# Kernel tuning notes

Measured on AMD Instinct MI355X. Metric: run time of the kernel, lower is better.

## Reference

```python
import jax, jax.numpy as jnp
import numpy as np

B, T = 64, 1000
RNN_DIM, EMB_DIM, ATT_DIM, LOC_DIM, KSIZE = 1024, 512, 128, 32, 31


def setup_inputs() -> dict:
    key = jax.random.key(0)
    ks = jax.random.split(key, 8)
    s = 0.02  # small init scale for weights
    return {
        "attention_hidden_state": jax.random.normal(ks[0], (B, RNN_DIM), jnp.float32),
        "memory": jax.random.normal(ks[1], (B, T, EMB_DIM), jnp.float32),
        "processed_memory": jax.random.normal(ks[2], (B, T, ATT_DIM), jnp.float32),
        "attention_weights_cat": jax.random.uniform(ks[3], (B, 2, T), jnp.float32),
        "mask": jnp.zeros((B, T), dtype=bool),
        "W_query": jax.random.normal(ks[4], (ATT_DIM, RNN_DIM), jnp.float32) * s,
        "conv_w": jax.random.normal(ks[5], (LOC_DIM, 2, KSIZE), jnp.float32) * s,
        "W_loc": jax.random.normal(ks[6], (ATT_DIM, LOC_DIM), jnp.float32) * s,
        "v": jax.random.normal(ks[7], (1, ATT_DIM), jnp.float32) * s,
    }


def reference(attention_hidden_state, memory, processed_memory,
              attention_weights_cat, mask, W_query, conv_w, W_loc, v):
    # processed_query: (B, 1, ATT_DIM)
    pq = (attention_hidden_state @ W_query.T)[:, None, :]
    # location features: conv1d over (B, 2, T), SAME padding, no bias
    loc = jax.lax.conv_general_dilated(
        attention_weights_cat, conv_w,
        window_strides=(1,), padding="SAME",
        dimension_numbers=("NCH", "OIH", "NCH"))  # (B, LOC_DIM, T)
    loc = jnp.einsum("bct,ac->bta", loc, W_loc)  # (B, T, ATT_DIM)
    # energies: v . tanh(pq + loc + processed_memory) -> (B, T)
    energy = jnp.einsum("bta,oa->bt", jnp.tanh(pq + loc + processed_memory), v)
    energy = jnp.where(mask, -jnp.inf, energy)
    attention_weights = jax.nn.softmax(energy, axis=1)  # (B, T)
    attention_context = jnp.einsum("bt,bte->be", attention_weights, memory)
    return attention_context, attention_weights
```

## Files before the change

### kernel.cpp

```cpp
#include <hip/hip_runtime.h>
#include <hip/hip_bf16.h>
#include <math.h>

#define B 64
#define T 1000
#define RNN_DIM 1024
#define EMB_DIM 512
#define ATT_DIM 128
#define LOC_DIM 32
#define KSIZE 31
#define PAD 15
#define ET 64
#define ESL 32

__global__ __launch_bounds__(256) void pq_kernel(
    const float* __restrict__ hidden,
    const float* __restrict__ Wq,
    float* __restrict__ pq)
{
    int gwave = (blockIdx.x * blockDim.x + threadIdx.x) >> 6;
    int lane  = threadIdx.x & 63;
    int b = gwave >> 7;
    int a = gwave & 127;

    const float4* h4 = (const float4*)(hidden + (size_t)b * RNN_DIM);
    const float4* w4 = (const float4*)(Wq + (size_t)a * RNN_DIM);

    float acc = 0.f;
#pragma unroll
    for (int j = 0; j < 4; ++j) {
        float4 h = h4[j * 64 + lane];
        float4 w = w4[j * 64 + lane];
        acc += h.x * w.x + h.y * w.y + h.z * w.z + h.w * w.w;
    }
#pragma unroll
    for (int off = 32; off > 0; off >>= 1)
        acc += __shfl_down(acc, off, 64);
    if (lane == 0) pq[gwave] = acc;
}

__global__ __launch_bounds__(256) void energy_kernel(
    const float* __restrict__ aw,
    const float* __restrict__ cw,
    const float* __restrict__ wl,
    const float* __restrict__ pq,
    const float* __restrict__ pm,
    const float* __restrict__ v,
    float* __restrict__ energy)
{
    __shared__ float aw_lds[2][ET + 2 * PAD];
    __shared__ float cw_lds[LOC_DIM][2][KSIZE];
    __shared__ float wl_lds[ATT_DIM][36];
    __shared__ float pq_lds[ATT_DIM];
    __shared__ float v_lds[ATT_DIM];
    __shared__ float loc_lds[ET][36];

    const int b   = blockIdx.x;
    const int t0  = blockIdx.y * ET;
    const int tid = threadIdx.x;

    const int TL = tid >> 4;
    const int AL = tid & 15;
    const int tb = TL * 4;

    float acc_e[4][8];
#pragma unroll
    for (int jj = 0; jj < 4; ++jj) {
        const int t = t0 + tb + jj;
        const bool ok = (t < T);
        const float* prow = pm + ((size_t)b * T + (ok ? t : 0)) * ATT_DIM + AL;
#pragma unroll
        for (int aa = 0; aa < 8; ++aa)
            acc_e[jj][aa] = ok ? prow[16 * aa] : 0.f;
    }

    for (int i = tid; i < LOC_DIM * 2 * KSIZE; i += 256)
        ((float*)cw_lds)[i] = cw[i];
    for (int i = tid; i < ATT_DIM * LOC_DIM; i += 256)
        wl_lds[i >> 5][i & 31] = wl[i];
    if (tid < ATT_DIM) {
        pq_lds[tid] = pq[b * ATT_DIM + tid];
        v_lds[tid]  = v[tid];
    }
    for (int i = tid; i < 2 * (ET + 2 * PAD); i += 256) {
        int ch = i / (ET + 2 * PAD);
        int p  = i % (ET + 2 * PAD);
        int t  = t0 + p - PAD;
        aw_lds[ch][p] = (t >= 0 && t < T) ? aw[(size_t)b * 2 * T + ch * T + t] : 0.f;
    }
    __syncthreads();

    {
        const int c  = tid & 31;
        const int tg = tid >> 5;
        float acc[8];
#pragma unroll
        for (int j = 0; j < 8; ++j) acc[j] = 0.f;
#pragma unroll
        for (int ch = 0; ch < 2; ++ch) {
            float awr[KSIZE + 7];
#pragma unroll
            for (int j = 0; j < KSIZE + 7; ++j) awr[j] = aw_lds[ch][tg * 8 + j];
#pragma unroll
            for (int k = 0; k < KSIZE; ++k) {
                float cv = cw_lds[c][ch][k];
#pragma unroll
                for (int j = 0; j < 8; ++j) acc[j] += cv * awr[k + j];
            }
        }
#pragma unroll
        for (int j = 0; j < 8; ++j) loc_lds[tg * 8 + j][c] = acc[j];
    }
    __syncthreads();

#pragma unroll
    for (int h = 0; h < 4; ++h) {
        float lrh[4][8];
#pragma unroll
        for (int jj = 0; jj < 4; ++jj) {
            *((float4*)&lrh[jj][0]) = *((const float4*)&loc_lds[tb + jj][8 * h]);
            *((float4*)&lrh[jj][4]) = *((const float4*)&loc_lds[tb + jj][8 * h + 4]);
        }
#pragma unroll
        for (int aa = 0; aa < 8; ++aa) {
            const int a = AL + 16 * aa;
            float4 w0 = *((const float4*)&wl_lds[a][8 * h]);
            float4 w1 = *((const float4*)&wl_lds[a][8 * h + 4]);
#pragma unroll
            for (int jj = 0; jj < 4; ++jj) {
                acc_e[jj][aa] +=
                      w0.x * lrh[jj][0] + w0.y * lrh[jj][1]
                    + w0.z * lrh[jj][2] + w0.w * lrh[jj][3]
                    + w1.x * lrh[jj][4] + w1.y * lrh[jj][5]
                    + w1.z * lrh[jj][6] + w1.w * lrh[jj][7];
            }
        }
    }

    float acc[4] = {0.f, 0.f, 0.f, 0.f};
#pragma unroll
    for (int aa = 0; aa < 8; ++aa) {
        const int a = AL + 16 * aa;
        const float pqa = pq_lds[a];
        const float va  = v_lds[a];
#pragma unroll
        for (int jj = 0; jj < 4; ++jj) {
            float e = acc_e[jj][aa] + pqa;
            float ex = __expf(2.f * e);
            float th = 1.f - 2.f * __builtin_amdgcn_rcpf(1.f + ex);
            acc[jj] += va * th;
        }
    }
#pragma unroll
    for (int jj = 0; jj < 4; ++jj) {
        float s = acc[jj];
        s += __shfl_xor(s, 1, 64);
        s += __shfl_xor(s, 2, 64);
        s += __shfl_xor(s, 4, 64);
        s += __shfl_xor(s, 8, 64);
        if (AL == 0) {
            int t = t0 + tb + jj;
            if (t < T) energy[b * T + t] = s;
        }
    }
}

__global__ __launch_bounds__(256) void softmax_context_kernel(
    const float* __restrict__ memory,
    const float* __restrict__ energy,
    const unsigned char* __restrict__ mask,
    float* __restrict__ out)
{
    __shared__ float w_lds[1024];
    __shared__ float sred[4];
    __shared__ float cred[4][ESL];

    const int b   = blockIdx.x;
    const int e0  = blockIdx.y * ESL;
    const int tid = threadIdx.x;
    const int col = tid & 7;
    const int rg  = tid >> 3;

    float e[4];
#pragma unroll
    for (int j = 0; j < 4; ++j) {
        int t = tid + j * 256;
        bool ok = (t < T);
        float val = ok ? energy[b * T + t] : -INFINITY;
        unsigned char m = ok ? mask[b * T + t] : (unsigned char)1;
        e[j] = (ok && !m) ? val : -INFINITY;
    }

    const float4* mem4 = (const float4*)(memory + (size_t)b * T * EMB_DIM + e0);
    float4 mA[8], mB[8];
#pragma unroll
    for (int u = 0; u < 8; ++u)
        mA[u] = mem4[(size_t)(rg + 32 * u) * 128 + col];

    float mx = fmaxf(fmaxf(e[0], e[1]), fmaxf(e[2], e[3]));
#pragma unroll
    for (int off = 32; off > 0; off >>= 1)
        mx = fmaxf(mx, __shfl_down(mx, off, 64));
    if ((tid & 63) == 0) sred[tid >> 6] = mx;
    __syncthreads();
    mx = fmaxf(fmaxf(sred[0], sred[1]), fmaxf(sred[2], sred[3]));
    __syncthreads();

    float sum = 0.f;
    float ex[4];
#pragma unroll
    for (int j = 0; j < 4; ++j) {
        ex[j] = (e[j] == -INFINITY) ? 0.f : __expf(e[j] - mx);
        sum += ex[j];
    }
#pragma unroll
    for (int off = 32; off > 0; off >>= 1)
        sum += __shfl_down(sum, off, 64);
    if ((tid & 63) == 0) sred[tid >> 6] = sum;
    __syncthreads();
    sum = sred[0] + sred[1] + sred[2] + sred[3];
    float inv = 1.f / sum;

#pragma unroll
    for (int j = 0; j < 4; ++j) {
        int t = tid + j * 256;
        float wv = ex[j] * inv;
        w_lds[t] = (t < T) ? wv : 0.f;
        if (blockIdx.y == 0 && t < T)
            out[B * EMB_DIM + b * T + t] = wv;
    }
    __syncthreads();

    float4 acc = {0.f, 0.f, 0.f, 0.f};

#define CTX_ISSUE(buf, base)                                              \
    _Pragma("unroll")                                                     \
    for (int u = 0; u < 8; ++u)                                           \
        buf[u] = mem4[(size_t)((base) + rg + 32 * u) * 128 + col];

#define CTX_ISSUE_CLAMP(buf, base)                                        \
    _Pragma("unroll")                                                     \
    for (int u = 0; u < 8; ++u) {                                         \
        int r  = (base) + rg + 32 * u;                                    \
        int rc = (r < T) ? r : (T - 1);                                   \
        buf[u] = mem4[(size_t)rc * 128 + col];                            \
    }

#define CTX_CONSUME(buf, base)                                            \
    _Pragma("unroll")                                                     \
    for (int u = 0; u < 8; ++u) {                                         \
        float wt = w_lds[(base) + rg + 32 * u];                           \
        acc.x += wt * buf[u].x; acc.y += wt * buf[u].y;                   \
        acc.z += wt * buf[u].z; acc.w += wt * buf[u].w;                   \
    }

    CTX_ISSUE(mB, 256)
    CTX_CONSUME(mA, 0)
    CTX_ISSUE(mA, 512)
    CTX_CONSUME(mB, 256)
    CTX_ISSUE_CLAMP(mB, 768)
    CTX_CONSUME(mA, 512)
    CTX_CONSUME(mB, 768)

#undef CTX_ISSUE
#undef CTX_ISSUE_CLAMP
#undef CTX_CONSUME

    acc.x += __shfl_xor(acc.x, 8, 64);  acc.x += __shfl_xor(acc.x, 16, 64);  acc.x += __shfl_xor(acc.x, 32, 64);
    acc.y += __shfl_xor(acc.y, 8, 64);  acc.y += __shfl_xor(acc.y, 16, 64);  acc.y += __shfl_xor(acc.y, 32, 64);
    acc.z += __shfl_xor(acc.z, 8, 64);  acc.z += __shfl_xor(acc.z, 16, 64);  acc.z += __shfl_xor(acc.z, 32, 64);
    acc.w += __shfl_xor(acc.w, 8, 64);  acc.w += __shfl_xor(acc.w, 16, 64);  acc.w += __shfl_xor(acc.w, 32, 64);

    if ((tid & 63) < 8)
        *((float4*)&cred[tid >> 6][4 * col]) = acc;
    __syncthreads();
    if (tid < ESL) {
        float s = cred[0][tid] + cred[1][tid] + cred[2][tid] + cred[3][tid];
        out[b * EMB_DIM + e0 + tid] = s;
    }
}

extern "C" void kernel_launch(void* const* d_in, const int* in_sizes, int n_in,
                              void* d_out, int out_size, void* d_ws, size_t ws_size,
                              hipStream_t stream) {
    const float* hidden = (const float*)d_in[0];
    const float* memory = (const float*)d_in[1];
    const float* pm     = (const float*)d_in[2];
    const float* aw     = (const float*)d_in[3];
    const unsigned char* mask = (const unsigned char*)d_in[4];
    const float* Wq     = (const float*)d_in[5];
    const float* cw     = (const float*)d_in[6];
    const float* wl     = (const float*)d_in[7];
    const float* v      = (const float*)d_in[8];

    float* out = (float*)d_out;

    float* pq_ws     = (float*)d_ws;
    float* energy_ws = pq_ws + B * ATT_DIM;

    pq_kernel<<<dim3((B * ATT_DIM) / 4), dim3(256), 0, stream>>>(hidden, Wq, pq_ws);

    energy_kernel<<<dim3(B, (T + ET - 1) / ET), dim3(256), 0, stream>>>(
        aw, cw, wl, pq_ws, pm, v, energy_ws);

    softmax_context_kernel<<<dim3(B, EMB_DIM / ESL), dim3(256), 0, stream>>>(
        memory, energy_ws, mask, out);
}
```

Before: 267.8 us.

## Compute location projection with split-bf16 MFMA instead of scalar FP32 FMAs

The loc·W_loc projection in the energy kernel moves from scalar FP32 FMAs to 16x16x32 bf16 MFMA instructions. Both operands are split into bf16 hi/lo parts and three MFMAs are issued to recover near-FP32 accuracy. The processed_memory load and the tanh/v reduction are remapped to the MFMA output layout. The change targets ALU time in the energy kernel. It adds conversion work and extra LDS arrays, and it may leave the kernel memory-bound, since the softmax/context kernel probably dominates.

```diff
diff --git a/kernel.cpp b/kernel.cpp
--- a/kernel.cpp
+++ b/kernel.cpp
@@ -12,6 +12,15 @@
 #define PAD 15
 #define ET 64
 #define ESL 32
+
+typedef __attribute__((ext_vector_type(4))) float f32x4;
+typedef __attribute__((ext_vector_type(8))) short bf16x8;
+
+__device__ inline unsigned short bf16_rne(float x) {
+    unsigned u = __float_as_uint(x);
+    u += 0x7fff + ((u >> 16) & 1);
+    return (unsigned short)(u >> 16);
+}
 
 __global__ __launch_bounds__(256) void pq_kernel(
     const float* __restrict__ hidden,
@@ -50,34 +59,31 @@
 {
     __shared__ float aw_lds[2][ET + 2 * PAD];
     __shared__ float cw_lds[LOC_DIM][2][KSIZE];
-    __shared__ float wl_lds[ATT_DIM][36];
+    __shared__ __align__(16) unsigned short wl_hi[ATT_DIM][LOC_DIM];
+    __shared__ __align__(16) unsigned short wl_lo[ATT_DIM][LOC_DIM];
+    __shared__ __align__(16) unsigned short loc_hi[ET][LOC_DIM];
+    __shared__ __align__(16) unsigned short loc_lo[ET][LOC_DIM];
     __shared__ float pq_lds[ATT_DIM];
     __shared__ float v_lds[ATT_DIM];
-    __shared__ float loc_lds[ET][36];
 
     const int b   = blockIdx.x;
     const int t0  = blockIdx.y * ET;
     const int tid = threadIdx.x;
 
-    const int TL = tid >> 4;
-    const int AL = tid & 15;
-    const int tb = TL * 4;
-
-    float acc_e[4][8];
-#pragma unroll
-    for (int jj = 0; jj < 4; ++jj) {
-        const int t = t0 + tb + jj;
-        const bool ok = (t < T);
-        const float* prow = pm + ((size_t)b * T + (ok ? t : 0)) * ATT_DIM + AL;
-#pragma unroll
-        for (int aa = 0; aa < 8; ++aa)
-            acc_e[jj][aa] = ok ? prow[16 * aa] : 0.f;
-    }
+    const int w   = tid >> 6;
+    const int l   = tid & 63;
+    const int c15 = l & 15;
+    const int g   = l >> 4;
 
     for (int i = tid; i < LOC_DIM * 2 * KSIZE; i += 256)
         ((float*)cw_lds)[i] = cw[i];
-    for (int i = tid; i < ATT_DIM * LOC_DIM; i += 256)
-        wl_lds[i >> 5][i & 31] = wl[i];
+    for (int i = tid; i < ATT_DIM * LOC_DIM; i += 256) {
+        float x = wl[i];
+        unsigned short h = bf16_rne(x);
+        float hf = __uint_as_float((unsigned)h << 16);
+        wl_hi[i >> 5][i & 31] = h;
+        wl_lo[i >> 5][i & 31] = bf16_rne(x - hf);
+    }
     if (tid < ATT_DIM) {
         pq_lds[tid] = pq[b * ATT_DIM + tid];
         v_lds[tid]  = v[tid];
@@ -93,9 +99,9 @@
     {
         const int c  = tid & 31;
         const int tg = tid >> 5;
-        float acc[8];
-#pragma unroll
-        for (int j = 0; j < 8; ++j) acc[j] = 0.f;
+        float cacc[8];
+#pragma unroll
+        for (int j = 0; j < 8; ++j) cacc[j] = 0.f;
 #pragma unroll
         for (int ch = 0; ch < 2; ++ch) {
             float awr[KSIZE + 7];
@@ -105,62 +111,75 @@
             for (int k = 0; k < KSIZE; ++k) {
                 float cv = cw_lds[c][ch][k];
 #pragma unroll
-                for (int j = 0; j < 8; ++j) acc[j] += cv * awr[k + j];
+                for (int j = 0; j < 8; ++j) cacc[j] += cv * awr[k + j];
             }
         }
 #pragma unroll
-        for (int j = 0; j < 8; ++j) loc_lds[tg * 8 + j][c] = acc[j];
-    }
-    __syncthreads();
-
-#pragma unroll
-    for (int h = 0; h < 4; ++h) {
-        float lrh[4][8];
-#pragma unroll
-        for (int jj = 0; jj < 4; ++jj) {
-            *((float4*)&lrh[jj][0]) = *((const float4*)&loc_lds[tb + jj][8 * h]);
-            *((float4*)&lrh[jj][4]) = *((const float4*)&loc_lds[tb + jj][8 * h + 4]);
-        }
-#pragma unroll
-        for (int aa = 0; aa < 8; ++aa) {
-            const int a = AL + 16 * aa;
-            float4 w0 = *((const float4*)&wl_lds[a][8 * h]);
-            float4 w1 = *((const float4*)&wl_lds[a][8 * h + 4]);
-#pragma unroll
-            for (int jj = 0; jj < 4; ++jj) {
-                acc_e[jj][aa] +=
-                      w0.x * lrh[jj][0] + w0.y * lrh[jj][1]
-                    + w0.z * lrh[jj][2] + w0.w * lrh[jj][3]
-                    + w1.x * lrh[jj][4] + w1.y * lrh[jj][5]
-                    + w1.z * lrh[jj][6] + w1.w * lrh[jj][7];
+        for (int j = 0; j < 8; ++j) {
+            float x = cacc[j];
+            unsigned short h = bf16_rne(x);
+            float hf = __uint_as_float((unsigned)h << 16);
+            loc_hi[tg * 8 + j][c] = h;
+            loc_lo[tg * 8 + j][c] = bf16_rne(x - hf);
+        }
+    }
+
+    f32x4 acc[8];
+    {
+        const float* pmb = pm + (size_t)b * T * ATT_DIM;
+        const int tbase = t0 + 16 * w + 4 * g;
+#pragma unroll
+        for (int n = 0; n < 8; ++n) {
+#pragma unroll
+            for (int r = 0; r < 4; ++r) {
+                int t = tbase + r;
+                acc[n][r] = (t < T) ? pmb[(size_t)t * ATT_DIM + 16 * n + c15] : 0.f;
             }
         }
     }
-
-    float acc[4] = {0.f, 0.f, 0.f, 0.f};
-#pragma unroll
-    for (int aa = 0; aa < 8; ++aa) {
-        const int a = AL + 16 * aa;
-        const float pqa = pq_lds[a];
-        const float va  = v_lds[a];
-#pragma unroll
-        for (int jj = 0; jj < 4; ++jj) {
-            float e = acc_e[jj][aa] + pqa;
-            float ex = __expf(2.f * e);
-            float th = 1.f - 2.f * __builtin_amdgcn_rcpf(1.f + ex);
-            acc[jj] += va * th;
-        }
-    }
-#pragma unroll
-    for (int jj = 0; jj < 4; ++jj) {
-        float s = acc[jj];
-        s += __shfl_xor(s, 1, 64);
-        s += __shfl_xor(s, 2, 64);
-        s += __shfl_xor(s, 4, 64);
-        s += __shfl_xor(s, 8, 64);
-        if (AL == 0) {
-            int t = t0 + tb + jj;
-            if (t < T) energy[b * T + t] = s;
+    __syncthreads();
+
+    {
+        bf16x8 aH = *(const bf16x8*)&loc_hi[16 * w + c15][8 * g];
+        bf16x8 aL = *(const bf16x8*)&loc_lo[16 * w + c15][8 * g];
+#pragma unroll
+        for (int n = 0; n < 8; ++n) {
+            bf16x8 bH = *(const bf16x8*)&wl_hi[16 * n + c15][8 * g];
+            bf16x8 bL = *(const bf16x8*)&wl_lo[16 * n + c15][8 * g];
+            acc[n] = __builtin_amdgcn_mfma_f32_16x16x32_bf16(aH, bH, acc[n], 0, 0, 0);
+            acc[n] = __builtin_amdgcn_mfma_f32_16x16x32_bf16(aH, bL, acc[n], 0, 0, 0);
+            acc[n] = __builtin_amdgcn_mfma_f32_16x16x32_bf16(aL, bH, acc[n], 0, 0, 0);
+        }
+    }
+
+    {
+        float s[4] = {0.f, 0.f, 0.f, 0.f};
+#pragma unroll
+        for (int n = 0; n < 8; ++n) {
+            const float pqa = pq_lds[16 * n + c15];
+            const float va  = v_lds[16 * n + c15];
+#pragma unroll
+            for (int r = 0; r < 4; ++r) {
+                float e = acc[n][r] + pqa;
+                float ex = __expf(2.f * e);
+                float th = 1.f - 2.f * __builtin_amdgcn_rcpf(1.f + ex);
+                s[r] += va * th;
+            }
+        }
+#pragma unroll
+        for (int r = 0; r < 4; ++r) {
+            s[r] += __shfl_xor(s[r], 1, 64);
+            s[r] += __shfl_xor(s[r], 2, 64);
+            s[r] += __shfl_xor(s[r], 4, 64);
+            s[r] += __shfl_xor(s[r], 8, 64);
+        }
+        if (c15 == 0) {
+            const int tbase = t0 + 16 * w + 4 * g;
+#pragma unroll
+            for (int r = 0; r < 4; ++r) {
+                int t = tbase + r;
+                if (t < T) energy[b * T + t] = s[r];
+            }
         }
     }
 }
```

After: 240.2 us. 10.3% less time.
